# Performance work log

Measured on AMD Instinct MI355X. Metric: run time of the kernel, lower is better.

## Reference

```python
import jax, jax.numpy as jnp
import numpy as np

NE, NR, D, B = 1_000_000, 1000, 32, 1_048_576
CURV = 1.0  # curvature K
HALF = D // 2


def _project(spatial):
    # recompute time component so point lies on hyperboloid <x,x>_L = -1/K
    x0 = jnp.sqrt(1.0 / CURV + jnp.sum(spatial * spatial, axis=-1, keepdims=True))
    return jnp.concatenate([x0, spatial], axis=-1)


def _lorentz_inner(u, v):
    return -u[..., 0] * v[..., 0] + jnp.sum(u[..., 1:] * v[..., 1:], axis=-1)


def setup_inputs() -> dict:
    key = jax.random.key(0)
    k0, k1, k2, k3, k4, k5, k6, k7 = jax.random.split(key, 8)
    tangent = jax.random.normal(k0, (NE, D), dtype=jnp.float32) * 0.01
    x0 = jnp.sqrt(1.0 / CURV + jnp.sum(tangent * tangent, axis=-1, keepdims=True))
    entity_emb = jnp.concatenate([x0, tangent], axis=-1)  # [NE, D+1]
    rel_boost_w = jax.random.normal(k1, (NR, D), dtype=jnp.float32) * 0.01
    rel_rot_w = jax.random.normal(k2, (NR, D), dtype=jnp.float32) * 0.01  # torch init is zeros; small noise for a nontrivial test
    rel_trans_w = jax.random.normal(k3, (NR, D), dtype=jnp.float32) * 0.01
    ent_bias_w = jax.random.normal(k4, (NE, 1), dtype=jnp.float32) * 0.01
    heads = jax.random.randint(k5, (B,), 0, NE)
    relations = jax.random.randint(k6, (B,), 0, NR)
    tails = jax.random.randint(k7, (B,), 0, NE)
    return {"heads": heads, "relations": relations, "tails": tails,
            "entity_emb": entity_emb, "rel_boost_w": rel_boost_w,
            "rel_rot_w": rel_rot_w, "rel_trans_w": rel_trans_w,
            "ent_bias_w": ent_bias_w}


def reference(heads, relations, tails, entity_emb, rel_boost_w, rel_rot_w, rel_trans_w, ent_bias_w):
    h = entity_emb[heads]                      # [B, D+1]
    t = entity_emb[tails]                      # [B, D+1]
    boost = rel_boost_w[relations]             # [B, D]
    rotation = rel_rot_w[relations]            # [B, D]
    translation = rel_trans_w[relations]       # [B, D]

    # --- spatial rotation: pairwise Givens rotations (i, i+HALF) ---
    x0 = h[..., 0:1]
    sp = h[..., 1:]
    a, b = sp[..., :HALF], sp[..., HALF:]
    c = jnp.cos(rotation[..., :HALF])
    s = jnp.sin(rotation[..., :HALF])
    rotated = jnp.concatenate([c * a - s * b, s * a + c * b], axis=-1)
    h_rot = jnp.concatenate([x0, rotated], axis=-1)

    # --- Lorentz boost along first spatial axis (only rapidity[..., 0] used) ---
    rap = jnp.clip(boost, -2.0, 2.0)
    c0 = jnp.cosh(rap[..., 0:1])
    s0 = jnp.sinh(rap[..., 0:1])
    bx0 = h_rot[..., 0:1]
    bx1 = h_rot[..., 1:2]
    new_x1 = bx0 * s0 + bx1 * c0
    new_spatial = jnp.concatenate([new_x1, h_rot[..., 2:]], axis=-1)
    h_boost = _project(new_spatial)  # time component recomputed by projection

    # --- exp map with tangent v = 0.1 * [0, translation] ---
    v = jnp.concatenate([jnp.zeros_like(translation[..., 0:1]), translation], axis=-1) * 0.1
    vn = jnp.sqrt(jnp.clip(_lorentz_inner(v, v), 1e-6, None))[..., None]
    res = jnp.cosh(vn) * h_boost + jnp.sinh(vn) * v / vn
    h_trans = _project(res[..., 1:])

    # --- Lorentz distance and score ---
    inner = _lorentz_inner(h_trans, t)
    ic = jnp.clip(-inner * CURV, 1.0 + 1e-6, None)
    dist = (1.0 / np.sqrt(CURV)) * jnp.arccosh(ic)
    b_h = ent_bias_w[heads][..., 0]
    b_t = ent_bias_w[tails][..., 0]
    return -dist * dist + b_h + b_t
```

## Files before the change

### kernel.cpp

```cpp
#include <hip/hip_runtime.h>
#include <hip/hip_fp16.h>
#include <math.h>

#define NR_ 1000
#define NE_ 1000000
#define D_ 32
#define HALF_ 16
#define EMB_DIM 33
#define TAB_STRIDE 68
#define H16_BYTES ((size_t)NE_ * 64)
#define REPACK_BLOCKS 15625

__global__ __launch_bounds__(256) void prep_kernel(
    const float* __restrict__ emb, const float* __restrict__ boost_w,
    const float* __restrict__ rot_w, const float* __restrict__ trans_w,
    unsigned int* __restrict__ h16, float* __restrict__ tab) {
  const int b = blockIdx.x;
  if (b < REPACK_BLOCKS) {
    int t = b * 256 + threadIdx.x;
    int r = t >> 2, q = t & 3;
    const float* pa = emb + (size_t)r * EMB_DIM + 1 + 4 * q;
    const float* pb = pa + HALF_;
    float a0 = __builtin_nontemporal_load(pa + 0);
    float a1 = __builtin_nontemporal_load(pa + 1);
    float a2 = __builtin_nontemporal_load(pa + 2);
    float a3 = __builtin_nontemporal_load(pa + 3);
    float b0 = __builtin_nontemporal_load(pb + 0);
    float b1 = __builtin_nontemporal_load(pb + 1);
    float b2 = __builtin_nontemporal_load(pb + 2);
    float b3 = __builtin_nontemporal_load(pb + 3);
    union { __half2 h; unsigned int u; } c0, c1, c2, c3;
    c0.h = __half2(__float2half_rn(a0), __float2half_rn(a1));
    c1.h = __half2(__float2half_rn(a2), __float2half_rn(a3));
    c2.h = __half2(__float2half_rn(b0), __float2half_rn(b1));
    c3.h = __half2(__float2half_rn(b2), __float2half_rn(b3));
    uint4 v = make_uint4(c0.u, c1.u, c2.u, c3.u);
    *reinterpret_cast<uint4*>(h16 + (size_t)r * 16 + 4 * q) = v;
    return;
  }
  int r = (b - REPACK_BLOCKS) * 256 + threadIdx.x;
  if (r >= NR_) return;
  const float* ro = rot_w   + (size_t)r * D_;
  const float* tr = trans_w + (size_t)r * D_;
  float* o = tab + (size_t)r * TAB_STRIDE;
  #pragma unroll
  for (int j = 0; j < HALF_; ++j) {
    float th = ro[j];
    o[j]         = cosf(th);
    o[HALF_ + j] = sinf(th);
  }
  float s2 = 0.f;
  #pragma unroll
  for (int j = 0; j < D_; ++j) { float v = tr[j]; s2 = fmaf(v, v, s2); }
  float vn  = sqrtf(fmaxf(0.01f * s2, 1e-6f));
  float k   = sinhf(vn) / vn * 0.1f;
  #pragma unroll
  for (int j = 0; j < D_; ++j) o[2 * HALF_ + j] = k * tr[j];
  float rap = fminf(fmaxf(boost_w[(size_t)r * D_], -2.f), 2.f);
  o[64] = coshf(rap);
  o[65] = sinhf(rap);
  o[66] = coshf(vn);
  o[67] = 0.f;
}

__global__ __launch_bounds__(256) void lorentz_coop_kernel(
    const int* __restrict__ heads, const int* __restrict__ rels,
    const int* __restrict__ tails, const unsigned int* __restrict__ h16,
    const float* __restrict__ bias, const float* __restrict__ tab,
    float* __restrict__ out, int n) {
  const int q = threadIdx.x & 3;
  const int e = (blockIdx.x * 256 + threadIdx.x) >> 2;
  const int i = (e < n) ? e : (n - 1);

  const int hd = heads[i];
  const int rl = rels[i];
  const int tl = tails[i];

  const uint4 hv = *reinterpret_cast<const uint4*>(h16 + (size_t)hd * 16 + 4 * q);
  const uint4 tv = *reinterpret_cast<const uint4*>(h16 + (size_t)tl * 16 + 4 * q);

  const float4* __restrict__ T =
      reinterpret_cast<const float4*>(tab + (size_t)rl * TAB_STRIDE);
  const float4 cq = T[q];
  const float4 sq = T[4 + q];
  const float4 ka = T[8 + q];
  const float4 kb = T[12 + q];
  const float4 hp = T[16];
  const float bsum = bias[hd] + bias[tl];

  union U2 { unsigned int u; __half2 h; };
  U2 u0, u1, u2, u3;
  u0.u = hv.x; u1.u = hv.y; u2.u = hv.z; u3.u = hv.w;
  const float2 fa01 = __half22float2(u0.h);
  const float2 fa23 = __half22float2(u1.h);
  const float2 fb01 = __half22float2(u2.h);
  const float2 fb23 = __half22float2(u3.h);
  const float a0 = fa01.x, a1 = fa01.y, a2 = fa23.x, a3 = fa23.y;
  const float b0 = fb01.x, b1 = fb01.y, b2 = fb23.x, b3 = fb23.y;

  float hsq = a0 * a0;
  hsq = fmaf(a1, a1, hsq); hsq = fmaf(a2, a2, hsq); hsq = fmaf(a3, a3, hsq);
  hsq = fmaf(b0, b0, hsq); hsq = fmaf(b1, b1, hsq);
  hsq = fmaf(b2, b2, hsq); hsq = fmaf(b3, b3, hsq);
  hsq += __shfl_xor(hsq, 1);
  hsq += __shfl_xor(hsq, 2);
  const float x0 = sqrtf(1.f + hsq);

  float rA0 = cq.x * a0 - sq.x * b0;
  float rA1 = cq.y * a1 - sq.y * b1;
  float rA2 = cq.z * a2 - sq.z * b2;
  float rA3 = cq.w * a3 - sq.w * b3;
  const float rB0 = fmaf(sq.x, a0, cq.x * b0);
  const float rB1 = fmaf(sq.y, a1, cq.y * b1);
  const float rB2 = fmaf(sq.z, a2, cq.z * b2);
  const float rB3 = fmaf(sq.w, a3, cq.w * b3);

  if (q == 0) rA0 = fmaf(x0, hp.y, rA0 * hp.x);
  const float cvn = hp.z;

  const float sA0 = fmaf(cvn, rA0, ka.x);
  const float sA1 = fmaf(cvn, rA1, ka.y);
  const float sA2 = fmaf(cvn, rA2, ka.z);
  const float sA3 = fmaf(cvn, rA3, ka.w);
  const float sB0 = fmaf(cvn, rB0, kb.x);
  const float sB1 = fmaf(cvn, rB1, kb.y);
  const float sB2 = fmaf(cvn, rB2, kb.z);
  const float sB3 = fmaf(cvn, rB3, kb.w);

  float n2 = sA0 * sA0;
  n2 = fmaf(sA1, sA1, n2); n2 = fmaf(sA2, sA2, n2); n2 = fmaf(sA3, sA3, n2);
  n2 = fmaf(sB0, sB0, n2); n2 = fmaf(sB1, sB1, n2);
  n2 = fmaf(sB2, sB2, n2); n2 = fmaf(sB3, sB3, n2);
  n2 += __shfl_xor(n2, 1);
  n2 += __shfl_xor(n2, 2);
  const float ht0 = sqrtf(1.f + n2);

  U2 w0, w1, w2, w3;
  w0.u = tv.x; w1.u = tv.y; w2.u = tv.z; w3.u = tv.w;
  const float2 ta01 = __half22float2(w0.h);
  const float2 ta23 = __half22float2(w1.h);
  const float2 tb01 = __half22float2(w2.h);
  const float2 tb23 = __half22float2(w3.h);

  float dot = sA0 * ta01.x;
  dot = fmaf(sA1, ta01.y, dot); dot = fmaf(sA2, ta23.x, dot);
  dot = fmaf(sA3, ta23.y, dot);
  dot = fmaf(sB0, tb01.x, dot); dot = fmaf(sB1, tb01.y, dot);
  dot = fmaf(sB2, tb23.x, dot); dot = fmaf(sB3, tb23.y, dot);

  float tsq = ta01.x * ta01.x;
  tsq = fmaf(ta01.y, ta01.y, tsq); tsq = fmaf(ta23.x, ta23.x, tsq);
  tsq = fmaf(ta23.y, ta23.y, tsq);
  tsq = fmaf(tb01.x, tb01.x, tsq); tsq = fmaf(tb01.y, tb01.y, tsq);
  tsq = fmaf(tb23.x, tb23.x, tsq); tsq = fmaf(tb23.y, tb23.y, tsq);

  dot += __shfl_xor(dot, 1);
  dot += __shfl_xor(dot, 2);
  tsq += __shfl_xor(tsq, 1);
  tsq += __shfl_xor(tsq, 2);
  const float t0 = sqrtf(1.f + tsq);

  const float neg_inner = fmaf(ht0, t0, -dot);
  const float ic = fmaxf(neg_inner, 1.0f + 1e-6f);
  const float dist = acoshf(ic);
  if (q == 0 && e < n) out[e] = bsum - dist * dist;
}

__global__ __launch_bounds__(256) void lorentz_fallback_kernel(
    const int* __restrict__ heads, const int* __restrict__ rels,
    const int* __restrict__ tails, const float* __restrict__ emb,
    const float* __restrict__ boost_w, const float* __restrict__ rot_w,
    const float* __restrict__ trans_w, const float* __restrict__ bias,
    float* __restrict__ out, int n) {
  int i = blockIdx.x * blockDim.x + threadIdx.x;
  if (i >= n) return;
  int hd = heads[i], rl = rels[i], tl = tails[i];
  const float* hrow = emb + (size_t)hd * EMB_DIM;
  const float* trow = emb + (size_t)tl * EMB_DIM;
  const float* ro = rot_w   + (size_t)rl * D_;
  const float* tr = trans_w + (size_t)rl * D_;
  float c[HALF_], s[HALF_], kt[D_];
  #pragma unroll
  for (int j = 0; j < HALF_; ++j) { float th = ro[j]; c[j] = cosf(th); s[j] = sinf(th); }
  float s2 = 0.f;
  #pragma unroll
  for (int j = 0; j < D_; ++j) { float v = tr[j]; s2 = fmaf(v, v, s2); }
  float vn = sqrtf(fmaxf(0.01f * s2, 1e-6f));
  float cvn = coshf(vn);
  float k = sinhf(vn) / vn * 0.1f;
  #pragma unroll
  for (int j = 0; j < D_; ++j) kt[j] = k * tr[j];
  float rap = fminf(fmaxf(boost_w[(size_t)rl * D_], -2.f), 2.f);
  float c0 = coshf(rap), s0 = sinhf(rap);
  float x0 = hrow[0];
  float r[D_];
  #pragma unroll
  for (int j = 0; j < HALF_; ++j) {
    float a = hrow[1 + j], b = hrow[1 + HALF_ + j];
    r[j] = c[j] * a - s[j] * b;
    r[HALF_ + j] = s[j] * a + c[j] * b;
  }
  r[0] = fmaf(x0, s0, r[0] * c0);
  float t0 = trow[0], n2 = 0.f, dot = 0.f;
  #pragma unroll
  for (int j = 0; j < D_; ++j) {
    float rsv = fmaf(cvn, r[j], kt[j]);
    n2  = fmaf(rsv, rsv, n2);
    dot = fmaf(rsv, trow[1 + j], dot);
  }
  float ht0 = sqrtf(1.f + n2);
  float neg_inner = fmaf(ht0, t0, -dot);
  float ic = fmaxf(neg_inner, 1.0f + 1e-6f);
  float dist = acoshf(ic);
  out[i] = bias[hd] + bias[tl] - dist * dist;
}

extern "C" void kernel_launch(void* const* d_in, const int* in_sizes, int n_in,
                              void* d_out, int out_size, void* d_ws, size_t ws_size,
                              hipStream_t stream) {
  const int*   heads  = (const int*)d_in[0];
  const int*   rels   = (const int*)d_in[1];
  const int*   tails  = (const int*)d_in[2];
  const float* emb    = (const float*)d_in[3];
  const float* boostw = (const float*)d_in[4];
  const float* rotw   = (const float*)d_in[5];
  const float* transw = (const float*)d_in[6];
  const float* bias   = (const float*)d_in[7];
  float* out = (float*)d_out;
  int n = in_sizes[0];

  const size_t tab_bytes = (size_t)NR_ * TAB_STRIDE * sizeof(float);
  dim3 block(256);

  if (ws_size >= H16_BYTES + tab_bytes) {
    unsigned int* h16 = (unsigned int*)d_ws;
    float* tab = (float*)((char*)d_ws + H16_BYTES);
    prep_kernel<<<dim3(REPACK_BLOCKS + 4), block, 0, stream>>>(
        emb, boostw, rotw, transw, h16, tab);
    dim3 grid_main((n + 63) / 64);
    lorentz_coop_kernel<<<grid_main, block, 0, stream>>>(
        heads, rels, tails, h16, bias, tab, out, n);
  } else {
    dim3 grid((n + 255) / 256);
    lorentz_fallback_kernel<<<grid, block, 0, stream>>>(
        heads, rels, tails, emb, boostw, rotw, transw, bias, out, n);
  }
}
```

Baseline: 280.6 us.

## Drop fp16 entity repack and gather fp32 embeddings directly in main kernel

Removes the per-call pass that converts all 1M entity rows to a packed fp16 table, which read about 132MB and wrote 64MB each call. The main kernel now gathers fp32 rows straight from the original 33-float embedding, reusing the stored time component instead of recomputing it from the spatial norm. The relation-table prep is spread over 4 threads per relation. In exchange, gathers are unaligned scalar loads of twice as many bytes per row, which may hurt gather efficiency.

```diff
diff --git a/kernel.cpp b/kernel.cpp
--- a/kernel.cpp
+++ b/kernel.cpp
@@ -1,5 +1,4 @@
 #include <hip/hip_runtime.h>
-#include <hip/hip_fp16.h>
 #include <math.h>
 
 #define NR_ 1000
@@ -8,64 +7,53 @@
 #define HALF_ 16
 #define EMB_DIM 33
 #define TAB_STRIDE 68
-#define H16_BYTES ((size_t)NE_ * 64)
-#define REPACK_BLOCKS 15625
-
-__global__ __launch_bounds__(256) void prep_kernel(
-    const float* __restrict__ emb, const float* __restrict__ boost_w,
-    const float* __restrict__ rot_w, const float* __restrict__ trans_w,
-    unsigned int* __restrict__ h16, float* __restrict__ tab) {
-  const int b = blockIdx.x;
-  if (b < REPACK_BLOCKS) {
-    int t = b * 256 + threadIdx.x;
-    int r = t >> 2, q = t & 3;
-    const float* pa = emb + (size_t)r * EMB_DIM + 1 + 4 * q;
-    const float* pb = pa + HALF_;
-    float a0 = __builtin_nontemporal_load(pa + 0);
-    float a1 = __builtin_nontemporal_load(pa + 1);
-    float a2 = __builtin_nontemporal_load(pa + 2);
-    float a3 = __builtin_nontemporal_load(pa + 3);
-    float b0 = __builtin_nontemporal_load(pb + 0);
-    float b1 = __builtin_nontemporal_load(pb + 1);
-    float b2 = __builtin_nontemporal_load(pb + 2);
-    float b3 = __builtin_nontemporal_load(pb + 3);
-    union { __half2 h; unsigned int u; } c0, c1, c2, c3;
-    c0.h = __half2(__float2half_rn(a0), __float2half_rn(a1));
-    c1.h = __half2(__float2half_rn(a2), __float2half_rn(a3));
-    c2.h = __half2(__float2half_rn(b0), __float2half_rn(b1));
-    c3.h = __half2(__float2half_rn(b2), __float2half_rn(b3));
-    uint4 v = make_uint4(c0.u, c1.u, c2.u, c3.u);
-    *reinterpret_cast<uint4*>(h16 + (size_t)r * 16 + 4 * q) = v;
-    return;
-  }
-  int r = (b - REPACK_BLOCKS) * 256 + threadIdx.x;
+
+__global__ __launch_bounds__(256) void tab_prep_kernel(
+    const float* __restrict__ boost_w, const float* __restrict__ rot_w,
+    const float* __restrict__ trans_w, float* __restrict__ tab) {
+  const int t = blockIdx.x * 256 + threadIdx.x;
+  const int r = t >> 2, q = t & 3;
   if (r >= NR_) return;
-  const float* ro = rot_w   + (size_t)r * D_;
-  const float* tr = trans_w + (size_t)r * D_;
+  const float* ro = rot_w   + (size_t)r * D_ + 4 * q;
+  const float* ta = trans_w + (size_t)r * D_ + 4 * q;
+  const float* tb = ta + HALF_;
   float* o = tab + (size_t)r * TAB_STRIDE;
-  #pragma unroll
-  for (int j = 0; j < HALF_; ++j) {
-    float th = ro[j];
-    o[j]         = cosf(th);
-    o[HALF_ + j] = sinf(th);
-  }
-  float s2 = 0.f;
-  #pragma unroll
-  for (int j = 0; j < D_; ++j) { float v = tr[j]; s2 = fmaf(v, v, s2); }
-  float vn  = sqrtf(fmaxf(0.01f * s2, 1e-6f));
-  float k   = sinhf(vn) / vn * 0.1f;
-  #pragma unroll
-  for (int j = 0; j < D_; ++j) o[2 * HALF_ + j] = k * tr[j];
-  float rap = fminf(fmaxf(boost_w[(size_t)r * D_], -2.f), 2.f);
-  o[64] = coshf(rap);
-  o[65] = sinhf(rap);
-  o[66] = coshf(vn);
-  o[67] = 0.f;
-}
-
-__global__ __launch_bounds__(256) void lorentz_coop_kernel(
+
+  float ta0 = ta[0], ta1 = ta[1], ta2 = ta[2], ta3 = ta[3];
+  float tb0 = tb[0], tb1 = tb[1], tb2 = tb[2], tb3 = tb[3];
+  float s2 = ta0 * ta0;
+  s2 = fmaf(ta1, ta1, s2); s2 = fmaf(ta2, ta2, s2); s2 = fmaf(ta3, ta3, s2);
+  s2 = fmaf(tb0, tb0, s2); s2 = fmaf(tb1, tb1, s2);
+  s2 = fmaf(tb2, tb2, s2); s2 = fmaf(tb3, tb3, s2);
+  s2 += __shfl_xor(s2, 1);
+  s2 += __shfl_xor(s2, 2);
+
+  float vn = sqrtf(fmaxf(0.01f * s2, 1e-6f));
+  float k  = sinhf(vn) / vn * 0.1f;
+
+  #pragma unroll
+  for (int m = 0; m < 4; ++m) {
+    float th = ro[m];
+    o[4 * q + m]         = cosf(th);
+    o[HALF_ + 4 * q + m] = sinf(th);
+  }
+  o[32 + 4 * q + 0] = k * ta0; o[32 + 4 * q + 1] = k * ta1;
+  o[32 + 4 * q + 2] = k * ta2; o[32 + 4 * q + 3] = k * ta3;
+  o[48 + 4 * q + 0] = k * tb0; o[48 + 4 * q + 1] = k * tb1;
+  o[48 + 4 * q + 2] = k * tb2; o[48 + 4 * q + 3] = k * tb3;
+
+  if (q == 0) {
+    float rap = fminf(fmaxf(boost_w[(size_t)r * D_], -2.f), 2.f);
+    o[64] = coshf(rap);
+    o[65] = sinhf(rap);
+    o[66] = coshf(vn);
+    o[67] = 0.f;
+  }
+}
+
+__global__ __launch_bounds__(256) void lorentz_direct_kernel(
     const int* __restrict__ heads, const int* __restrict__ rels,
-    const int* __restrict__ tails, const unsigned int* __restrict__ h16,
+    const int* __restrict__ tails, const float* __restrict__ emb,
     const float* __restrict__ bias, const float* __restrict__ tab,
     float* __restrict__ out, int n) {
   const int q = threadIdx.x & 3;
@@ -76,8 +64,19 @@
   const int rl = rels[i];
   const int tl = tails[i];
 
-  const uint4 hv = *reinterpret_cast<const uint4*>(h16 + (size_t)hd * 16 + 4 * q);
-  const uint4 tv = *reinterpret_cast<const uint4*>(h16 + (size_t)tl * 16 + 4 * q);
+  const float* __restrict__ hrow = emb + (size_t)hd * EMB_DIM;
+  const float* __restrict__ trow = emb + (size_t)tl * EMB_DIM;
+
+  const float hx0 = hrow[0];
+  const float a0 = hrow[1 + 4 * q], a1 = hrow[2 + 4 * q],
+              a2 = hrow[3 + 4 * q], a3 = hrow[4 + 4 * q];
+  const float b0 = hrow[17 + 4 * q], b1 = hrow[18 + 4 * q],
+              b2 = hrow[19 + 4 * q], b3 = hrow[20 + 4 * q];
+  const float tx0 = trow[0];
+  const float ta0 = trow[1 + 4 * q], ta1 = trow[2 + 4 * q],
+              ta2 = trow[3 + 4 * q], ta3 = trow[4 + 4 * q];
+  const float tb0 = trow[17 + 4 * q], tb1 = trow[18 + 4 * q],
+              tb2 = trow[19 + 4 * q], tb3 = trow[20 + 4 * q];
 
   const float4* __restrict__ T =
       reinterpret_cast<const float4*>(tab + (size_t)rl * TAB_STRIDE);
@@ -88,24 +87,6 @@
   const float4 hp = T[16];
   const float bsum = bias[hd] + bias[tl];
 
-  union U2 { unsigned int u; __half2 h; };
-  U2 u0, u1, u2, u3;
-  u0.u = hv.x; u1.u = hv.y; u2.u = hv.z; u3.u = hv.w;
-  const float2 fa01 = __half22float2(u0.h);
-  const float2 fa23 = __half22float2(u1.h);
-  const float2 fb01 = __half22float2(u2.h);
-  const float2 fb23 = __half22float2(u3.h);
-  const float a0 = fa01.x, a1 = fa01.y, a2 = fa23.x, a3 = fa23.y;
-  const float b0 = fb01.x, b1 = fb01.y, b2 = fb23.x, b3 = fb23.y;
-
-  float hsq = a0 * a0;
-  hsq = fmaf(a1, a1, hsq); hsq = fmaf(a2, a2, hsq); hsq = fmaf(a3, a3, hsq);
-  hsq = fmaf(b0, b0, hsq); hsq = fmaf(b1, b1, hsq);
-  hsq = fmaf(b2, b2, hsq); hsq = fmaf(b3, b3, hsq);
-  hsq += __shfl_xor(hsq, 1);
-  hsq += __shfl_xor(hsq, 2);
-  const float x0 = sqrtf(1.f + hsq);
-
   float rA0 = cq.x * a0 - sq.x * b0;
   float rA1 = cq.y * a1 - sq.y * b1;
   float rA2 = cq.z * a2 - sq.z * b2;
@@ -115,7 +96,7 @@
   const float rB2 = fmaf(sq.z, a2, cq.z * b2);
   const float rB3 = fmaf(sq.w, a3, cq.w * b3);
 
-  if (q == 0) rA0 = fmaf(x0, hp.y, rA0 * hp.x);
+  if (q == 0) rA0 = fmaf(hx0, hp.y, rA0 * hp.x);
   const float cvn = hp.z;
 
   const float sA0 = fmaf(cvn, rA0, ka.x);
@@ -131,36 +112,20 @@
   n2 = fmaf(sA1, sA1, n2); n2 = fmaf(sA2, sA2, n2); n2 = fmaf(sA3, sA3, n2);
   n2 = fmaf(sB0, sB0, n2); n2 = fmaf(sB1, sB1, n2);
   n2 = fmaf(sB2, sB2, n2); n2 = fmaf(sB3, sB3, n2);
-  n2 += __shfl_xor(n2, 1);
-  n2 += __shfl_xor(n2, 2);
+
+  float dot = sA0 * ta0;
+  dot = fmaf(sA1, ta1, dot); dot = fmaf(sA2, ta2, dot);
+  dot = fmaf(sA3, ta3, dot);
+  dot = fmaf(sB0, tb0, dot); dot = fmaf(sB1, tb1, dot);
+  dot = fmaf(sB2, tb2, dot); dot = fmaf(sB3, tb3, dot);
+
+  n2  += __shfl_xor(n2, 1);
+  dot += __shfl_xor(dot, 1);
+  n2  += __shfl_xor(n2, 2);
+  dot += __shfl_xor(dot, 2);
+
   const float ht0 = sqrtf(1.f + n2);
-
-  U2 w0, w1, w2, w3;
-  w0.u = tv.x; w1.u = tv.y; w2.u = tv.z; w3.u = tv.w;
-  const float2 ta01 = __half22float2(w0.h);
-  const float2 ta23 = __half22float2(w1.h);
-  const float2 tb01 = __half22float2(w2.h);
-  const float2 tb23 = __half22float2(w3.h);
-
-  float dot = sA0 * ta01.x;
-  dot = fmaf(sA1, ta01.y, dot); dot = fmaf(sA2, ta23.x, dot);
-  dot = fmaf(sA3, ta23.y, dot);
-  dot = fmaf(sB0, tb01.x, dot); dot = fmaf(sB1, tb01.y, dot);
-  dot = fmaf(sB2, tb23.x, dot); dot = fmaf(sB3, tb23.y, dot);
-
-  float tsq = ta01.x * ta01.x;
-  tsq = fmaf(ta01.y, ta01.y, tsq); tsq = fmaf(ta23.x, ta23.x, tsq);
-  tsq = fmaf(ta23.y, ta23.y, tsq);
-  tsq = fmaf(tb01.x, tb01.x, tsq); tsq = fmaf(tb01.y, tb01.y, tsq);
-  tsq = fmaf(tb23.x, tb23.x, tsq); tsq = fmaf(tb23.y, tb23.y, tsq);
-
-  dot += __shfl_xor(dot, 1);
-  dot += __shfl_xor(dot, 2);
-  tsq += __shfl_xor(tsq, 1);
-  tsq += __shfl_xor(tsq, 2);
-  const float t0 = sqrtf(1.f + tsq);
-
-  const float neg_inner = fmaf(ht0, t0, -dot);
+  const float neg_inner = fmaf(ht0, tx0, -dot);
   const float ic = fmaxf(neg_inner, 1.0f + 1e-6f);
   const float dist = acoshf(ic);
   if (q == 0 && e < n) out[e] = bsum - dist * dist;
@@ -232,14 +197,13 @@
   const size_t tab_bytes = (size_t)NR_ * TAB_STRIDE * sizeof(float);
   dim3 block(256);
 
-  if (ws_size >= H16_BYTES + tab_bytes) {
-    unsigned int* h16 = (unsigned int*)d_ws;
-    float* tab = (float*)((char*)d_ws + H16_BYTES);
-    prep_kernel<<<dim3(REPACK_BLOCKS + 4), block, 0, stream>>>(
-        emb, boostw, rotw, transw, h16, tab);
+  if (ws_size >= tab_bytes) {
+    float* tab = (float*)d_ws;
+    tab_prep_kernel<<<dim3((NR_ * 4 + 255) / 256), block, 0, stream>>>(
+        boostw, rotw, transw, tab);
     dim3 grid_main((n + 63) / 64);
-    lorentz_coop_kernel<<<grid_main, block, 0, stream>>>(
-        heads, rels, tails, h16, bias, tab, out, n);
+    lorentz_direct_kernel<<<grid_main, block, 0, stream>>>(
+        heads, rels, tails, emb, bias, tab, out, n);
   } else {
     dim3 grid((n + 255) / 256);
     lorentz_fallback_kernel<<<grid, block, 0, stream>>>(
```

Result: no change. 281.5 us (+0.3%).
